# Kernel tuning notes

Hardware: AMD Instinct MI355X
Metric: run time of the kernel (lower is better)

The kernel has to match this reference:

```python
import jax, jax.numpy as jnp
import numpy as np

H = 1024   # hidden_size
NH = 32    # num_heads
D = H // NH  # head_dim = 32
M = 2      # num_timescales
BMIN, BMAX = 0.85, 0.9995
EPS = 1e-6
ROPE_BASE = 10000.0
LN_EPS = 1e-5


def setup_inputs() -> dict:
    key = jax.random.key(0)
    ks = jax.random.split(key, 8)
    b, t = 4, 1024
    x = jax.random.normal(ks[0], (b, t, H), jnp.float32)
    # xavier-uniform for q/k/v/out (matches _reset_parameters)
    sc = (6.0 / (H + H)) ** 0.5
    Wq = jax.random.uniform(ks[1], (H, H), jnp.float32, -sc, sc)
    Wk = jax.random.uniform(ks[2], (H, H), jnp.float32, -sc, sc)
    Wv = jax.random.uniform(ks[3], (H, H), jnp.float32, -sc, sc)
    Wout = jax.random.uniform(ks[4], (H, H), jnp.float32, -sc, sc)
    bout = jnp.zeros((H,), jnp.float32)
    # beta_proj: random weight, bias set so sigmoid(bias) = linspace(beta_min, beta_max)
    scb = (6.0 / (H + NH * M)) ** 0.5
    Wbeta = jax.random.uniform(ks[5], (NH * M, H), jnp.float32, -scb, scb)
    targets = jnp.linspace(BMIN, BMAX, M)
    bbeta = jnp.tile(jnp.log(targets / (1.0 - targets)), NH)  # repeat 'm -> (h m)'
    # mix_proj initialized to zeros (uniform mixing via softmax)
    Wmix = jnp.zeros((NH * M, H), jnp.float32)
    bmix = jnp.zeros((NH * M,), jnp.float32)
    ln_g = jnp.ones((H,), jnp.float32)
    ln_b = jnp.zeros((H,), jnp.float32)
    return dict(x=x, Wq=Wq, Wk=Wk, Wv=Wv, Wbeta=Wbeta, bbeta=bbeta,
                Wmix=Wmix, bmix=bmix, Wout=Wout, bout=bout, ln_g=ln_g, ln_b=ln_b)


def _rope(u, cos, sin):
    # u: [b,t,h,d] with d even; cos/sin: [1,t,1,d//2]
    half = D // 2
    u1, u2 = u[..., :half], u[..., half:]
    return jnp.concatenate([u1 * cos - u2 * sin, u1 * sin + u2 * cos], axis=-1)


def _forward(x, Wq, Wk, Wv, Wbeta, bbeta, Wmix, bmix, Wout, bout, ln_g, ln_b):
    b, t, _ = x.shape
    q = (x @ Wq.T).reshape(b, t, NH, D)
    k = (x @ Wk.T).reshape(b, t, NH, D)
    v = (x @ Wv.T).reshape(b, t, NH, D)
    # RoPE cache
    half = D // 2
    inv_freq = 1.0 / (ROPE_BASE ** (jnp.arange(half, dtype=jnp.float32) / half))
    freqs = jnp.arange(t, dtype=jnp.float32)[:, None] * inv_freq  # [t,half]
    cos = jnp.cos(freqs)[None, :, None, :]
    sin = jnp.sin(freqs)[None, :, None, :]
    q = _rope(q, cos, sin)
    k = _rope(k, cos, sin)
    phi_q = jax.nn.elu(q) + 1.0
    phi_k = jax.nn.elu(k) + 1.0
    beta = jnp.clip(jax.nn.sigmoid((x @ Wbeta.T + bbeta).reshape(b, t, NH, M)), BMIN, BMAX)
    mix = jax.nn.softmax((x @ Wmix.T + bmix).reshape(b, t, NH, M), axis=-1)

    def step(carry, xs):
        S, K = carry  # S:[b,h,M,d,d]  K:[b,h,M,d]
        pq, pk, vt, bt, mt = xs  # [b,h,d],[b,h,d],[b,h,d],[b,h,M],[b,h,M]
        K = K * bt[..., None] + pk[:, :, None, :]
        S = S * bt[..., None, None] + pk[:, :, None, :, None] * vt[:, :, None, None, :]
        num = jnp.einsum('bhd,bhmdc->bhmc', pq, S)
        den = jnp.einsum('bhd,bhmd->bhm', pq, K) + EPS
        y = jnp.sum(num / den[..., None] * mt[..., None], axis=2)  # [b,h,d]
        return (S, K), y

    S0 = jnp.zeros((b, NH, M, D, D), x.dtype)
    K0 = jnp.zeros((b, NH, M, D), x.dtype)
    tf = lambda a: jnp.moveaxis(a, 1, 0)  # time-major for scan
    _, ys = jax.lax.scan(step, (S0, K0), (tf(phi_q), tf(phi_k), tf(v), tf(beta), tf(mix)))
    y = jnp.moveaxis(ys, 0, 1).reshape(b, t, H) @ Wout.T + bout
    z = x + y  # residual; dropout is identity in eval
    mu = z.mean(-1, keepdims=True)
    var = ((z - mu) ** 2).mean(-1, keepdims=True)
    return (z - mu) / jnp.sqrt(var + LN_EPS) * ln_g + ln_b


def reference(x, Wq, Wk, Wv, Wbeta, bbeta, Wmix, bmix, Wout, bout, ln_g, ln_b):
    return _forward(x, Wq, Wk, Wv, Wbeta, bbeta, Wmix, bmix, Wout, bout, ln_g, ln_b)
```

## Files before the change

### kernel.cpp

```cpp
#include <hip/hip_runtime.h>
#include <math.h>

#define TT 1024
#define BB 4
#define HH 1024
#define NHH 32
#define CL 64
#define NCH (TT/CL)

typedef unsigned short u16;
typedef __attribute__((ext_vector_type(8))) short short8;
typedef __attribute__((ext_vector_type(8))) unsigned short u16x8;
typedef __attribute__((ext_vector_type(4))) float floatx4;

__device__ __forceinline__ float sigmoidf_(float x){ return 1.f/(1.f+expf(-x)); }
__device__ __forceinline__ u16 f2b(float f){
  union { float f; unsigned u; } x; x.f = f;
  unsigned r = x.u + 0x7FFFu + ((x.u >> 16) & 1u);
  return (u16)(r >> 16);
}
__device__ __forceinline__ float b2f(u16 v){
  union { unsigned u; float f; } x; x.u = ((unsigned)v) << 16;
  return x.f;
}

__global__ __launch_bounds__(256) void cast_all_k(
    const float* __restrict__ x, const float* __restrict__ Wq, const float* __restrict__ Wk,
    const float* __restrict__ Wv, const float* __restrict__ Wbeta, const float* __restrict__ Wmix,
    const float* __restrict__ Wout,
    u16* __restrict__ x_bf, u16* __restrict__ Wf, u16* __restrict__ Wout_bf)
{
  size_t e = ((size_t)blockIdx.x*256 + threadIdx.x)*4;
  const float* src; u16* dst; size_t so, dof;
  if      (e < 4194304) { src=x;     dst=x_bf;    so=e;          dof=so; }
  else if (e < 5242880) { src=Wq;    dst=Wf;      so=e-4194304;  dof=so; }
  else if (e < 6291456) { src=Wk;    dst=Wf;      so=e-5242880;  dof=so+1048576; }
  else if (e < 7340032) { src=Wv;    dst=Wf;      so=e-6291456;  dof=so+2097152; }
  else if (e < 7405568) { src=Wbeta; dst=Wf;      so=e-7340032;  dof=so+3145728; }
  else if (e < 7471104) { src=Wmix;  dst=Wf;      so=e-7405568;  dof=so+3211264; }
  else                  { src=Wout;  dst=Wout_bf; so=e-7471104;  dof=so; }
  float4 f = *reinterpret_cast<const float4*>(src + so);
  ushort4 u; u.x=f2b(f.x); u.y=f2b(f.y); u.z=f2b(f.z); u.w=f2b(f.w);
  *reinterpret_cast<ushort4*>(dst + dof) = u;
}

__global__ __launch_bounds__(256) void rope_table_k(float* __restrict__ ct, float* __restrict__ st){
  int idx = blockIdx.x*256 + threadIdx.x;
  int t = idx >> 4, j = idx & 15;
  float invf = powf(10000.f, -(float)j/16.f);
  float ang = (float)t * invf;
  ct[idx] = cosf(ang);
  st[idx] = sinf(ang);
}

__global__ __launch_bounds__(256) void gemm_qkv_k(
    const u16* __restrict__ A, const u16* __restrict__ W,
    const float* __restrict__ ct, const float* __restrict__ st,
    u16* __restrict__ qkv, float* __restrict__ bmraw)
{
  __shared__ u16 As[128*64];
  __shared__ u16 Ws[128*64];
  const int tid = threadIdx.x;
  const int lane = tid & 63;
  const int wave = tid >> 6;
  const int wm = wave >> 1, wn = wave & 1;
  const int row0 = blockIdx.y*128, col0 = blockIdx.x*128;
  const int lr = lane & 15, lkg = lane >> 4;

  floatx4 acc[4][4];
  #pragma unroll
  for (int mt=0; mt<4; ++mt)
    #pragma unroll
    for (int nt=0; nt<4; ++nt)
      acc[mt][nt] = (floatx4){0.f,0.f,0.f,0.f};

  for (int k0 = 0; k0 < 1024; k0 += 64) {
    __syncthreads();
    #pragma unroll
    for (int it = 0; it < 4; ++it) {
      int li  = it*256 + tid;
      int row = li >> 3, ckp = li & 7;
      int ck  = ckp ^ (row & 7);
      const u16* ga = A + (size_t)(row0+row)*1024 + k0 + ck*8;
      const u16* gw = W + (size_t)(col0+row)*1024 + k0 + ck*8;
      __builtin_amdgcn_global_load_lds(
          (const __attribute__((address_space(1))) void*)ga,
          (__attribute__((address_space(3))) void*)(As + (size_t)(li & ~63)*8), 16, 0, 0);
      __builtin_amdgcn_global_load_lds(
          (const __attribute__((address_space(1))) void*)gw,
          (__attribute__((address_space(3))) void*)(Ws + (size_t)(li & ~63)*8), 16, 0, 0);
    }
    __syncthreads();
    #pragma unroll
    for (int kk = 0; kk < 64; kk += 32) {
      short8 af[4], wf[4];
      const int ckw = (kk >> 3) + lkg;
      #pragma unroll
      for (int t = 0; t < 4; ++t) {
        int rowA = wm*64 + t*16 + lr;
        int rowW = wn*64 + t*16 + lr;
        af[t] = *reinterpret_cast<const short8*>(As + rowA*64 + (ckw ^ (rowA & 7))*8);
        wf[t] = *reinterpret_cast<const short8*>(Ws + rowW*64 + (ckw ^ (rowW & 7))*8);
      }
      #pragma unroll
      for (int mt = 0; mt < 4; ++mt)
        #pragma unroll
        for (int nt = 0; nt < 4; ++nt)
          acc[mt][nt] = __builtin_amdgcn_mfma_f32_16x16x32_bf16(af[mt], wf[nt], acc[mt][nt], 0, 0, 0);
    }
  }
  const int bx = blockIdx.x;
  if (bx < 16) {
    #pragma unroll
    for (int mt = 0; mt < 4; ++mt) {
      #pragma unroll
      for (int r = 0; r < 4; ++r) {
        int row = row0 + wm*64 + mt*16 + lkg*4 + r;
        int t = row & (TT-1);
        float c_ = ct[t*16 + lr], s_ = st[t*16 + lr];
        #pragma unroll
        for (int nt = 0; nt < 4; nt += 2) {
          float u1 = acc[mt][nt][r], u2 = acc[mt][nt+1][r];
          float r1 = u1*c_ - u2*s_;
          float r2 = u1*s_ + u2*c_;
          r1 = r1 > 0.f ? r1+1.f : expf(r1);
          r2 = r2 > 0.f ? r2+1.f : expf(r2);
          int col = col0 + wn*64 + nt*16 + lr;
          qkv[(size_t)row*3072 + col]      = f2b(r1);
          qkv[(size_t)row*3072 + col + 16] = f2b(r2);
        }
      }
    }
  } else if (bx < 24) {
    #pragma unroll
    for (int mt = 0; mt < 4; ++mt)
      #pragma unroll
      for (int r = 0; r < 4; ++r) {
        int row = row0 + wm*64 + mt*16 + lkg*4 + r;
        #pragma unroll
        for (int nt = 0; nt < 4; ++nt) {
          int col = col0 + wn*64 + nt*16 + lr;
          qkv[(size_t)row*3072 + col] = f2b(acc[mt][nt][r]);
        }
      }
  } else {
    #pragma unroll
    for (int mt = 0; mt < 4; ++mt)
      #pragma unroll
      for (int r = 0; r < 4; ++r) {
        int row = row0 + wm*64 + mt*16 + lkg*4 + r;
        #pragma unroll
        for (int nt = 0; nt < 4; ++nt) {
          int col = col0 + wn*64 + nt*16 + lr - 3072;
          bmraw[(size_t)row*128 + col] = acc[mt][nt][r];
        }
      }
  }
}

__global__ __launch_bounds__(256) void gemm_mfma_k(
    const u16* __restrict__ A, const u16* __restrict__ W,
    const float* __restrict__ bias, const float* __restrict__ res,
    float* __restrict__ Cf, int N, int K)
{
  __shared__ u16 As[128*64];
  __shared__ u16 Ws[128*64];
  const int tid = threadIdx.x;
  const int lane = tid & 63;
  const int wave = tid >> 6;
  const int wm = wave >> 1, wn = wave & 1;
  const int row0 = blockIdx.y*128, col0 = blockIdx.x*128;
  const int lr = lane & 15, lkg = lane >> 4;
  floatx4 acc[4][4];
  #pragma unroll
  for (int mt=0; mt<4; ++mt)
    #pragma unroll
    for (int nt=0; nt<4; ++nt)
      acc[mt][nt] = (floatx4){0.f,0.f,0.f,0.f};
  for (int k0 = 0; k0 < K; k0 += 64) {
    __syncthreads();
    #pragma unroll
    for (int it = 0; it < 4; ++it) {
      int li  = it*256 + tid;
      int row = li >> 3, ckp = li & 7;
      int ck  = ckp ^ (row & 7);
      const u16* ga = A + (size_t)(row0+row)*K + k0 + ck*8;
      const u16* gw = W + (size_t)(col0+row)*K + k0 + ck*8;
      __builtin_amdgcn_global_load_lds(
          (const __attribute__((address_space(1))) void*)ga,
          (__attribute__((address_space(3))) void*)(As + (size_t)(li & ~63)*8), 16, 0, 0);
      __builtin_amdgcn_global_load_lds(
          (const __attribute__((address_space(1))) void*)gw,
          (__attribute__((address_space(3))) void*)(Ws + (size_t)(li & ~63)*8), 16, 0, 0);
    }
    __syncthreads();
    #pragma unroll
    for (int kk = 0; kk < 64; kk += 32) {
      short8 af[4], wf[4];
      const int ckw = (kk >> 3) + lkg;
      #pragma unroll
      for (int t = 0; t < 4; ++t) {
        int rowA = wm*64 + t*16 + lr;
        int rowW = wn*64 + t*16 + lr;
        af[t] = *reinterpret_cast<const short8*>(As + rowA*64 + (ckw ^ (rowA & 7))*8);
        wf[t] = *reinterpret_cast<const short8*>(Ws + rowW*64 + (ckw ^ (rowW & 7))*8);
      }
      #pragma unroll
      for (int mt = 0; mt < 4; ++mt)
        #pragma unroll
        for (int nt = 0; nt < 4; ++nt)
          acc[mt][nt] = __builtin_amdgcn_mfma_f32_16x16x32_bf16(af[mt], wf[nt], acc[mt][nt], 0, 0, 0);
    }
  }
  #pragma unroll
  for (int mt = 0; mt < 4; ++mt) {
    #pragma unroll
    for (int r = 0; r < 4; ++r) {
      int row = row0 + wm*64 + mt*16 + lkg*4 + r;
      #pragma unroll
      for (int nt = 0; nt < 4; ++nt) {
        int col = col0 + wn*64 + nt*16 + lr;
        float v = acc[mt][nt][r];
        if (bias) v += bias[col];
        if (res)  v += res[(size_t)row*N + col];
        Cf[(size_t)row*N + col] = v;
      }
    }
  }
}

__global__ __launch_bounds__(256) void scan_delta_k(
    const u16* __restrict__ qkv, const float* __restrict__ bmraw,
    const float* __restrict__ bbeta,
    float* __restrict__ dS, float* __restrict__ dK,
    float* __restrict__ pLg, float* __restrict__ pg)
{
  __shared__ __align__(16) u16 K2T[2][32][72];
  __shared__ __align__(16) u16 VT[32][72];
  __shared__ float bets[2][64], pbuf[2][64], wjs[2][64], pLs[2];
  const int ch = blockIdx.x, h = blockIdx.y, b = blockIdx.z;
  const int bh = b*NHH + h;
  const int tid = threadIdx.x;
  const int t0 = ch*CL;
  const int j = tid >> 2, oct = tid & 3;
  size_t rowbase = (size_t)(b*TT + t0 + j)*3072 + h*32 + oct*8;
  u16x8 k8 = *reinterpret_cast<const u16x8*>(qkv + rowbase + 1024);
  u16x8 v8 = *reinterpret_cast<const u16x8*>(qkv + rowbase + 2048);
  if (tid < 128) {
    int m = tid & 1, tl = tid >> 1;
    float bv = bmraw[(size_t)(b*TT + t0 + tl)*128 + h*2 + m] + bbeta[h*2 + m];
    bets[m][tl] = fminf(fmaxf(sigmoidf_(bv), 0.85f), 0.9995f);
  }
  #pragma unroll
  for (int dd = 0; dd < 8; ++dd) VT[oct*8+dd][j] = v8[dd];
  __syncthreads();
  if (tid < 128) {
    int m = tid >> 6, l = tid & 63;
    float p = bets[m][l];
    #pragma unroll
    for (int off = 1; off < 64; off <<= 1) {
      float o = __shfl_up(p, off);
      if (l >= off) p *= o;
    }
    pbuf[m][l] = p;
    if (l == 63) pLs[m] = p;
  }
  __syncthreads();
  if (tid < 128) {
    int m = tid >> 6, l = tid & 63;
    wjs[m][l] = pLs[m] / pbuf[m][l];
    pg[(((size_t)bh*NCH + ch)*2 + m)*64 + l] = pbuf[m][l];
  }
  if (tid < 2) pLg[((size_t)bh*NCH + ch)*2 + tid] = pLs[tid];
  __syncthreads();
  float w0 = wjs[0][j], w1 = wjs[1][j];
  #pragma unroll
  for (int dd = 0; dd < 8; ++dd) {
    float kv = b2f(k8[dd]);
    K2T[0][oct*8+dd][j] = f2b(kv*w0);
    K2T[1][oct*8+dd][j] = f2b(kv*w1);
  }
  __syncthreads();
  {
    const int wv = tid >> 6, lane = tid & 63, lr = lane & 15, kg = lane >> 4;
    const int m = wv >> 1, mt = wv & 1;
    floatx4 a0 = (floatx4){0.f,0.f,0.f,0.f}, a1 = (floatx4){0.f,0.f,0.f,0.f};
    #pragma unroll
    for (int ks = 0; ks < 2; ++ks) {
      short8 af = *reinterpret_cast<const short8*>(&K2T[m][mt*16 + lr][ks*32 + kg*8]);
      short8 b0 = *reinterpret_cast<const short8*>(&VT[lr][ks*32 + kg*8]);
      short8 b1 = *reinterpret_cast<const short8*>(&VT[16 + lr][ks*32 + kg*8]);
      a0 = __builtin_amdgcn_mfma_f32_16x16x32_bf16(af, b0, a0, 0, 0, 0);
      a1 = __builtin_amdgcn_mfma_f32_16x16x32_bf16(af, b1, a1, 0, 0, 0);
    }
    size_t base = (((size_t)bh*NCH + ch)*2 + m)*1024;
    #pragma unroll
    for (int r = 0; r < 4; ++r) {
      int d = mt*16 + kg*4 + r;
      dS[base + d*32 + lr]      = a0[r];
      dS[base + d*32 + 16 + lr] = a1[r];
    }
  }
  if (tid < 64) {
    int m = tid >> 5, d = tid & 31;
    float s = 0.f;
    #pragma unroll
    for (int g = 0; g < 8; ++g) {
      u16x8 kk = *reinterpret_cast<const u16x8*>(&K2T[m][d][g*8]);
      #pragma unroll
      for (int dd = 0; dd < 8; ++dd) s += b2f(kk[dd]);
    }
    dK[(((size_t)bh*NCH + ch)*2 + m)*32 + d] = s;
  }
}

__global__ __launch_bounds__(1024) void scan_state_k(
    float* dSS0, float* dKK0, const float* __restrict__ pLg)
{
  const int bhm = blockIdx.x;
  const int bh = bhm >> 1, m = bhm & 1;
  const int tid = threadIdx.x;
  float pls[NCH], dv[NCH];
  #pragma unroll
  for (int ch = 0; ch < NCH; ++ch) pls[ch] = pLg[((size_t)bh*NCH + ch)*2 + m];
  #pragma unroll
  for (int ch = 0; ch < NCH; ++ch) dv[ch] = dSS0[(((size_t)bh*NCH + ch)*2 + m)*1024 + tid];
  float S = 0.f;
  #pragma unroll
  for (int ch = 0; ch < NCH; ++ch) {
    dSS0[(((size_t)bh*NCH + ch)*2 + m)*1024 + tid] = S;
    S = fmaf(pls[ch], S, dv[ch]);
  }
  if (tid < 32) {
    float kv[NCH];
    #pragma unroll
    for (int ch = 0; ch < NCH; ++ch) kv[ch] = dKK0[(((size_t)bh*NCH + ch)*2 + m)*32 + tid];
    float K0 = 0.f;
    #pragma unroll
    for (int ch = 0; ch < NCH; ++ch) {
      dKK0[(((size_t)bh*NCH + ch)*2 + m)*32 + tid] = K0;
      K0 = fmaf(pls[ch], K0, kv[ch]);
    }
  }
}

__global__ __launch_bounds__(256) void scan_apply_k(
    const u16* __restrict__ qkv, const float* __restrict__ bmraw,
    const float* __restrict__ bmix,
    const float* __restrict__ S0g, const float* __restrict__ K0g,
    const float* __restrict__ pg, u16* __restrict__ yb)
{
  __shared__ __align__(16) u16 Qs[64][32], Ks[64][32];
  __shared__ __align__(16) u16 VT[32][72];
  __shared__ __align__(16) u16 At[2][64][72];
  __shared__ __align__(16) u16 S0T[2][2][32][40];
  __shared__ float K0s[2][32];
  __shared__ float pbv[2][64], ipb[2][64], mixs[2][64], coef[2][64];
  const int ch = blockIdx.x, h = blockIdx.y, b = blockIdx.z;
  const int bh = b*NHH + h;
  const int tid = threadIdx.x;
  const int t0 = ch*CL;
  {
    int j = tid >> 2, oct = tid & 3;
    size_t rb = (size_t)(b*TT + t0 + j)*3072 + h*32 + oct*8;
    u16x8 q8 = *reinterpret_cast<const u16x8*>(qkv + rb);
    u16x8 k8 = *reinterpret_cast<const u16x8*>(qkv + rb + 1024);
    u16x8 v8 = *reinterpret_cast<const u16x8*>(qkv + rb + 2048);
    *reinterpret_cast<u16x8*>(&Qs[j][oct*8]) = q8;
    *reinterpret_cast<u16x8*>(&Ks[j][oct*8]) = k8;
    #pragma unroll
    for (int dd = 0; dd < 8; ++dd) VT[oct*8+dd][j] = v8[dd];
  }
  for (int u = tid; u < 2048; u += 256) {
    int m = u >> 10, r = u & 1023, d = r >> 5, c = r & 31;
    float val = S0g[(((size_t)bh*NCH + ch)*2 + m)*1024 + r];
    u16 hv = f2b(val);
    float lo = val - b2f(hv);
    S0T[m][0][c][d] = hv;
    S0T[m][1][c][d] = f2b(lo);
  }
  if (tid < 64) {
    int m = tid >> 5, d = tid & 31;
    K0s[m][d] = K0g[(((size_t)bh*NCH + ch)*2 + m)*32 + d];
  }
  if (tid < 128) {
    int m = tid & 1, i = tid >> 1;
    float p = pg[(((size_t)bh*NCH + ch)*2 + m)*64 + i];
    pbv[m][i] = p;
    ipb[m][i] = 1.f/p;
  } else if (tid < 192) {
    int i = tid - 128;
    size_t rb = (size_t)(b*TT + t0 + i)*128 + 64 + h*2;
    float a0 = bmraw[rb]   + bmix[h*2];
    float a1 = bmraw[rb+1] + bmix[h*2+1];
    float mx = fmaxf(a0, a1);
    float e0 = expf(a0-mx), e1 = expf(a1-mx);
    float inv = 1.f/(e0+e1);
    mixs[0][i] = e0*inv; mixs[1][i] = e1*inv;
  }
  __syncthreads();
  {
    const int wv = tid >> 6, lane = tid & 63, lr = lane & 15, kg = lane >> 4;
    short8 aq = *reinterpret_cast<const short8*>(&Qs[wv*16 + lr][kg*8]);
    #pragma unroll
    for (int nt = 0; nt < 4; ++nt) {
      short8 bk = *reinterpret_cast<const short8*>(&Ks[nt*16 + lr][kg*8]);
      floatx4 a0 = (floatx4){0.f,0.f,0.f,0.f};
      a0 = __builtin_amdgcn_mfma_f32_16x16x32_bf16(aq, bk, a0, 0, 0, 0);
      int jg = nt*16 + lr;
      float ip0 = ipb[0][jg], ip1 = ipb[1][jg];
      #pragma unroll
      for (int r = 0; r < 4; ++r) {
        int ig = wv*16 + kg*4 + r;
        float val = a0[r];
        bool ok = (jg <= ig);
        At[0][ig][jg] = f2b(ok ? val*ip0 : 0.f);
        At[1][ig][jg] = f2b(ok ? val*ip1 : 0.f);
      }
    }
  }
  __syncthreads();
  if (tid < 128) {
    int m = tid & 1, i = tid >> 1;
    float qK0 = 0.f;
    #pragma unroll
    for (int g = 0; g < 4; ++g) {
      u16x8 qq = *reinterpret_cast<const u16x8*>(&Qs[i][g*8]);
      #pragma unroll
      for (int dd = 0; dd < 8; ++dd) qK0 = fmaf(b2f(qq[dd]), K0s[m][g*8+dd], qK0);
    }
    float As_ = 0.f;
    #pragma unroll
    for (int g = 0; g < 8; ++g) {
      u16x8 aa = *reinterpret_cast<const u16x8*>(&At[m][i][g*8]);
      #pragma unroll
      for (int dd = 0; dd < 8; ++dd) As_ += b2f(aa[dd]);
    }
    float den = pbv[m][i]*(qK0 + As_) + 1e-6f;
    coef[m][i] = mixs[m][i]*pbv[m][i]/den;
  }
  __syncthreads();
  {
    const int wv = tid >> 6, lane = tid & 63, lr = lane & 15, kg = lane >> 4;
    const int i0 = wv*16;
    floatx4 accY[2][2];
    #pragma unroll
    for (int m = 0; m < 2; ++m)
      #pragma unroll
      for (int nt = 0; nt < 2; ++nt)
        accY[m][nt] = (floatx4){0.f,0.f,0.f,0.f};
    short8 aq = *reinterpret_cast<const short8*>(&Qs[i0 + lr][kg*8]);
    #pragma unroll
    for (int m = 0; m < 2; ++m)
      #pragma unroll
      for (int nt = 0; nt < 2; ++nt) {
        short8 bhi = *reinterpret_cast<const short8*>(&S0T[m][0][nt*16 + lr][kg*8]);
        short8 blo = *reinterpret_cast<const short8*>(&S0T[m][1][nt*16 + lr][kg*8]);
        accY[m][nt] = __builtin_amdgcn_mfma_f32_16x16x32_bf16(aq, bhi, accY[m][nt], 0, 0, 0);
        accY[m][nt] = __builtin_amdgcn_mfma_f32_16x16x32_bf16(aq, blo, accY[m][nt], 0, 0, 0);
      }
    #pragma unroll
    for (int ks = 0; ks < 2; ++ks) {
      short8 a0f = *reinterpret_cast<const short8*>(&At[0][i0 + lr][ks*32 + kg*8]);
      short8 a1f = *reinterpret_cast<const short8*>(&At[1][i0 + lr][ks*32 + kg*8]);
      short8 b0 = *reinterpret_cast<const short8*>(&VT[lr][ks*32 + kg*8]);
      short8 b1 = *reinterpret_cast<const short8*>(&VT[16 + lr][ks*32 + kg*8]);
      accY[0][0] = __builtin_amdgcn_mfma_f32_16x16x32_bf16(a0f, b0, accY[0][0], 0, 0, 0);
      accY[0][1] = __builtin_amdgcn_mfma_f32_16x16x32_bf16(a0f, b1, accY[0][1], 0, 0, 0);
      accY[1][0] = __builtin_amdgcn_mfma_f32_16x16x32_bf16(a1f, b0, accY[1][0], 0, 0, 0);
      accY[1][1] = __builtin_amdgcn_mfma_f32_16x16x32_bf16(a1f, b1, accY[1][1], 0, 0, 0);
    }
    #pragma unroll
    for (int r = 0; r < 4; ++r) {
      int i = i0 + kg*4 + r;
      float c0 = coef[0][i], c1 = coef[1][i];
      size_t ob = (size_t)(b*TT + t0 + i)*HH + h*32;
      yb[ob + lr]      = f2b(c0*accY[0][0][r] + c1*accY[1][0][r]);
      yb[ob + 16 + lr] = f2b(c0*accY[0][1][r] + c1*accY[1][1][r]);
    }
  }
}

__global__ __launch_bounds__(256) void ln_k(
    const float* __restrict__ z, const float* __restrict__ g,
    const float* __restrict__ bta, float* __restrict__ out)
{
  const int row = blockIdx.x;
  const int tid = threadIdx.x;
  const float* zr = z + (size_t)row*HH;
  float4 zv = reinterpret_cast<const float4*>(zr)[tid];
  float sum = zv.x+zv.y+zv.z+zv.w;
  float sq  = zv.x*zv.x + zv.y*zv.y + zv.z*zv.z + zv.w*zv.w;
  #pragma unroll
  for (int off=1; off<64; off<<=1){ sum += __shfl_xor(sum, off); sq += __shfl_xor(sq, off); }
  __shared__ float s1[4], s2[4];
  int w = tid>>6;
  if ((tid&63)==0){ s1[w]=sum; s2[w]=sq; }
  __syncthreads();
  sum = s1[0]+s1[1]+s1[2]+s1[3];
  sq  = s2[0]+s2[1]+s2[2]+s2[3];
  float mu  = sum * (1.f/1024.f);
  float var = sq * (1.f/1024.f) - mu*mu;
  float rstd = rsqrtf(var + 1e-5f);
  float4 gv = reinterpret_cast<const float4*>(g)[tid];
  float4 bv = reinterpret_cast<const float4*>(bta)[tid];
  float4 ov;
  ov.x = (zv.x-mu)*rstd*gv.x + bv.x;
  ov.y = (zv.y-mu)*rstd*gv.y + bv.y;
  ov.z = (zv.z-mu)*rstd*gv.z + bv.z;
  ov.w = (zv.w-mu)*rstd*gv.w + bv.w;
  reinterpret_cast<float4*>(out + (size_t)row*HH)[tid] = ov;
}

extern "C" void kernel_launch(void* const* d_in, const int* in_sizes, int n_in,
                              void* d_out, int out_size, void* d_ws, size_t ws_size,
                              hipStream_t stream)
{
  const float* x     = (const float*)d_in[0];
  const float* Wq    = (const float*)d_in[1];
  const float* Wk    = (const float*)d_in[2];
  const float* Wv    = (const float*)d_in[3];
  const float* Wbeta = (const float*)d_in[4];
  const float* bbeta = (const float*)d_in[5];
  const float* Wmix  = (const float*)d_in[6];
  const float* bmix  = (const float*)d_in[7];
  const float* Wout  = (const float*)d_in[8];
  const float* bout  = (const float*)d_in[9];
  const float* ln_g  = (const float*)d_in[10];
  const float* ln_b  = (const float*)d_in[11];
  float* out = (float*)d_out;

  float* ws = (float*)d_ws;
  float* ct      = ws;
  float* st      = ws + 16384;
  u16*   x_bf    = (u16*)(ws + 32768);
  u16*   Wf      = (u16*)(ws + 2129920);
  u16*   Wout_bf = (u16*)(ws + 3768320);
  u16*   qkv     = (u16*)(ws + 4292608);
  float* bmraw   = ws + 10584064;
  float* dSS0    = ws + 11108352;
  float* dKK0    = ws + 15302656;
  float* pLg     = ws + 15433728;
  float* pg      = ws + 15437824;
  u16*   y_bf    = x_bf;
  float* z       = dSS0;

  cast_all_k<<<8320, 256, 0, stream>>>(x, Wq, Wk, Wv, Wbeta, Wmix, Wout, x_bf, Wf, Wout_bf);
  rope_table_k<<<64, 256, 0, stream>>>(ct, st);
  gemm_qkv_k<<<dim3(25, 32), 256, 0, stream>>>(x_bf, Wf, ct, st, qkv, bmraw);
  dim3 gscan(NCH, 32, 4);
  scan_delta_k<<<gscan, 256, 0, stream>>>(qkv, bmraw, bbeta, dSS0, dKK0, pLg, pg);
  scan_state_k<<<256, 1024, 0, stream>>>(dSS0, dKK0, pLg);
  scan_apply_k<<<gscan, 256, 0, stream>>>(qkv, bmraw, bmix, dSS0, dKK0, pg, y_bf);
  gemm_mfma_k<<<dim3(8, 32), 256, 0, stream>>>(y_bf, Wout_bf, bout, x, z, 1024, 1024);
  ln_k<<<4096, 256, 0, stream>>>(z, ln_g, ln_b, out);
}
```

Before: 237.9 us.

## Fuse rope table into cast, split-K output GEMM, fold beta/mix into QKV epilogue

Merges the RoPE table kernel into the cast kernel, and computes beta sigmoid/clamp and the mix softmax in the QKV GEMM epilogue instead of in the scan kernels. The output projection is split-K into two halves writing separate partial buffers, and the residual, bias and partial sums are combined inside the layernorm kernel. It also reorders the GEMM block indexing into a 1D grid with row-fastest order and splits scan_state into 256-thread blocks. This removes one launch and redundant per-chunk beta/mix math, and doubles output-GEMM block count for better CU occupancy, at the cost of extra partial-buffer traffic.

```diff
diff --git a/kernel.cpp b/kernel.cpp
--- a/kernel.cpp
+++ b/kernel.cpp
@@ -28,9 +28,18 @@
     const float* __restrict__ x, const float* __restrict__ Wq, const float* __restrict__ Wk,
     const float* __restrict__ Wv, const float* __restrict__ Wbeta, const float* __restrict__ Wmix,
     const float* __restrict__ Wout,
-    u16* __restrict__ x_bf, u16* __restrict__ Wf, u16* __restrict__ Wout_bf)
-{
-  size_t e = ((size_t)blockIdx.x*256 + threadIdx.x)*4;
+    u16* __restrict__ x_bf, u16* __restrict__ Wf, u16* __restrict__ Wout_bf,
+    float* __restrict__ ct, float* __restrict__ st)
+{
+  int gid = blockIdx.x*256 + threadIdx.x;
+  if (gid < 16384) {
+    int t = gid >> 4, j = gid & 15;
+    float invf = powf(10000.f, -(float)j/16.f);
+    float ang = (float)t * invf;
+    ct[gid] = cosf(ang);
+    st[gid] = sinf(ang);
+  }
+  size_t e = (size_t)gid*4;
   const float* src; u16* dst; size_t so, dof;
   if      (e < 4194304) { src=x;     dst=x_bf;    so=e;          dof=so; }
   else if (e < 5242880) { src=Wq;    dst=Wf;      so=e-4194304;  dof=so; }
@@ -44,19 +53,11 @@
   *reinterpret_cast<ushort4*>(dst + dof) = u;
 }
 
-__global__ __launch_bounds__(256) void rope_table_k(float* __restrict__ ct, float* __restrict__ st){
-  int idx = blockIdx.x*256 + threadIdx.x;
-  int t = idx >> 4, j = idx & 15;
-  float invf = powf(10000.f, -(float)j/16.f);
-  float ang = (float)t * invf;
-  ct[idx] = cosf(ang);
-  st[idx] = sinf(ang);
-}
-
 __global__ __launch_bounds__(256) void gemm_qkv_k(
     const u16* __restrict__ A, const u16* __restrict__ W,
     const float* __restrict__ ct, const float* __restrict__ st,
-    u16* __restrict__ qkv, float* __restrict__ bmraw)
+    const float* __restrict__ bbeta, const float* __restrict__ bmix,
+    u16* __restrict__ qkv, float* __restrict__ betag, float* __restrict__ mixg)
 {
   __shared__ u16 As[128*64];
   __shared__ u16 Ws[128*64];
@@ -64,7 +65,8 @@
   const int lane = tid & 63;
   const int wave = tid >> 6;
   const int wm = wave >> 1, wn = wave & 1;
-  const int row0 = blockIdx.y*128, col0 = blockIdx.x*128;
+  const int id = blockIdx.x;
+  const int row0 = (id & 31)*128, bx = id >> 5, col0 = bx*128;
   const int lr = lane & 15, lkg = lane >> 4;
 
   floatx4 acc[4][4];
@@ -109,7 +111,6 @@
           acc[mt][nt] = __builtin_amdgcn_mfma_f32_16x16x32_bf16(af[mt], wf[nt], acc[mt][nt], 0, 0, 0);
     }
   }
-  const int bx = blockIdx.x;
   if (bx < 16) {
     #pragma unroll
     for (int mt = 0; mt < 4; ++mt) {
@@ -151,17 +152,26 @@
         int row = row0 + wm*64 + mt*16 + lkg*4 + r;
         #pragma unroll
         for (int nt = 0; nt < 4; ++nt) {
-          int col = col0 + wn*64 + nt*16 + lr - 3072;
-          bmraw[(size_t)row*128 + col] = acc[mt][nt][r];
+          int cidx = nt*16 + lr;
+          float v = acc[mt][nt][r];
+          if (wn == 0) {
+            float bv = sigmoidf_(v + bbeta[cidx]);
+            betag[(size_t)row*64 + cidx] = fminf(fmaxf(bv, 0.85f), 0.9995f);
+          } else {
+            float a = v + bmix[cidx];
+            float o = __shfl_xor(a, 1);
+            float e = expf(a - fmaxf(a, o));
+            float es = e + __shfl_xor(e, 1);
+            mixg[(size_t)row*64 + cidx] = e/es;
+          }
         }
       }
   }
 }
 
-__global__ __launch_bounds__(256) void gemm_mfma_k(
+__global__ __launch_bounds__(256) void gemm_out_k(
     const u16* __restrict__ A, const u16* __restrict__ W,
-    const float* __restrict__ bias, const float* __restrict__ res,
-    float* __restrict__ Cf, int N, int K)
+    float* __restrict__ Zp0, float* __restrict__ Zp1)
 {
   __shared__ u16 As[128*64];
   __shared__ u16 Ws[128*64];
@@ -169,7 +179,9 @@
   const int lane = tid & 63;
   const int wave = tid >> 6;
   const int wm = wave >> 1, wn = wave & 1;
-  const int row0 = blockIdx.y*128, col0 = blockIdx.x*128;
+  const int id = blockIdx.x;
+  const int row0 = (id & 31)*128, col0 = ((id >> 5) & 7)*128, kh = id >> 8;
+  float* Z = kh ? Zp1 : Zp0;
   const int lr = lane & 15, lkg = lane >> 4;
   floatx4 acc[4][4];
   #pragma unroll
@@ -177,15 +189,15 @@
     #pragma unroll
     for (int nt=0; nt<4; ++nt)
       acc[mt][nt] = (floatx4){0.f,0.f,0.f,0.f};
-  for (int k0 = 0; k0 < K; k0 += 64) {
+  for (int k0 = kh*512; k0 < kh*512 + 512; k0 += 64) {
     __syncthreads();
     #pragma unroll
     for (int it = 0; it < 4; ++it) {
       int li  = it*256 + tid;
       int row = li >> 3, ckp = li & 7;
       int ck  = ckp ^ (row & 7);
-      const u16* ga = A + (size_t)(row0+row)*K + k0 + ck*8;
-      const u16* gw = W + (size_t)(col0+row)*K + k0 + ck*8;
+      const u16* ga = A + (size_t)(row0+row)*1024 + k0 + ck*8;
+      const u16* gw = W + (size_t)(col0+row)*1024 + k0 + ck*8;
       __builtin_amdgcn_global_load_lds(
           (const __attribute__((address_space(1))) void*)ga,
           (__attribute__((address_space(3))) void*)(As + (size_t)(li & ~63)*8), 16, 0, 0);
@@ -213,25 +225,20 @@
     }
   }
   #pragma unroll
-  for (int mt = 0; mt < 4; ++mt) {
+  for (int mt = 0; mt < 4; ++mt)
     #pragma unroll
     for (int r = 0; r < 4; ++r) {
       int row = row0 + wm*64 + mt*16 + lkg*4 + r;
       #pragma unroll
       for (int nt = 0; nt < 4; ++nt) {
         int col = col0 + wn*64 + nt*16 + lr;
-        float v = acc[mt][nt][r];
-        if (bias) v += bias[col];
-        if (res)  v += res[(size_t)row*N + col];
-        Cf[(size_t)row*N + col] = v;
-      }
-    }
-  }
+        Z[(size_t)row*HH + col] = acc[mt][nt][r];
+      }
+    }
 }
 
 __global__ __launch_bounds__(256) void scan_delta_k(
-    const u16* __restrict__ qkv, const float* __restrict__ bmraw,
-    const float* __restrict__ bbeta,
+    const u16* __restrict__ qkv, const float* __restrict__ betag,
     float* __restrict__ dS, float* __restrict__ dK,
     float* __restrict__ pLg, float* __restrict__ pg)
 {
@@ -248,8 +255,7 @@
   u16x8 v8 = *reinterpret_cast<const u16x8*>(qkv + rowbase + 2048);
   if (tid < 128) {
     int m = tid & 1, tl = tid >> 1;
-    float bv = bmraw[(size_t)(b*TT + t0 + tl)*128 + h*2 + m] + bbeta[h*2 + m];
-    bets[m][tl] = fminf(fmaxf(sigmoidf_(bv), 0.85f), 0.9995f);
+    bets[m][tl] = betag[(size_t)(b*TT + t0 + tl)*64 + h*2 + m];
   }
   #pragma unroll
   for (int dd = 0; dd < 8; ++dd) VT[oct*8+dd][j] = v8[dd];
@@ -314,39 +320,39 @@
   }
 }
 
-__global__ __launch_bounds__(1024) void scan_state_k(
+__global__ __launch_bounds__(256) void scan_state_k(
     float* dSS0, float* dKK0, const float* __restrict__ pLg)
 {
-  const int bhm = blockIdx.x;
+  const int bhm = blockIdx.x >> 2, part = blockIdx.x & 3;
   const int bh = bhm >> 1, m = bhm & 1;
-  const int tid = threadIdx.x;
+  const int idx = part*256 + threadIdx.x;
   float pls[NCH], dv[NCH];
   #pragma unroll
   for (int ch = 0; ch < NCH; ++ch) pls[ch] = pLg[((size_t)bh*NCH + ch)*2 + m];
   #pragma unroll
-  for (int ch = 0; ch < NCH; ++ch) dv[ch] = dSS0[(((size_t)bh*NCH + ch)*2 + m)*1024 + tid];
+  for (int ch = 0; ch < NCH; ++ch) dv[ch] = dSS0[(((size_t)bh*NCH + ch)*2 + m)*1024 + idx];
   float S = 0.f;
   #pragma unroll
   for (int ch = 0; ch < NCH; ++ch) {
-    dSS0[(((size_t)bh*NCH + ch)*2 + m)*1024 + tid] = S;
+    dSS0[(((size_t)bh*NCH + ch)*2 + m)*1024 + idx] = S;
     S = fmaf(pls[ch], S, dv[ch]);
   }
-  if (tid < 32) {
+  if (part == 0 && threadIdx.x < 32) {
+    int d = threadIdx.x;
     float kv[NCH];
     #pragma unroll
-    for (int ch = 0; ch < NCH; ++ch) kv[ch] = dKK0[(((size_t)bh*NCH + ch)*2 + m)*32 + tid];
+    for (int ch = 0; ch < NCH; ++ch) kv[ch] = dKK0[(((size_t)bh*NCH + ch)*2 + m)*32 + d];
     float K0 = 0.f;
     #pragma unroll
     for (int ch = 0; ch < NCH; ++ch) {
-      dKK0[(((size_t)bh*NCH + ch)*2 + m)*32 + tid] = K0;
+      dKK0[(((size_t)bh*NCH + ch)*2 + m)*32 + d] = K0;
       K0 = fmaf(pls[ch], K0, kv[ch]);
     }
   }
 }
 
 __global__ __launch_bounds__(256) void scan_apply_k(
-    const u16* __restrict__ qkv, const float* __restrict__ bmraw,
-    const float* __restrict__ bmix,
+    const u16* __restrict__ qkv, const float* __restrict__ mixg,
     const float* __restrict__ S0g, const float* __restrict__ K0g,
     const float* __restrict__ pg, u16* __restrict__ yb)
 {
@@ -390,13 +396,9 @@
     ipb[m][i] = 1.f/p;
   } else if (tid < 192) {
     int i = tid - 128;
-    size_t rb = (size_t)(b*TT + t0 + i)*128 + 64 + h*2;
-    float a0 = bmraw[rb]   + bmix[h*2];
-    float a1 = bmraw[rb+1] + bmix[h*2+1];
-    float mx = fmaxf(a0, a1);
-    float e0 = expf(a0-mx), e1 = expf(a1-mx);
-    float inv = 1.f/(e0+e1);
-    mixs[0][i] = e0*inv; mixs[1][i] = e1*inv;
+    size_t rb = (size_t)(b*TT + t0 + i)*64 + h*2;
+    mixs[0][i] = mixg[rb];
+    mixs[1][i] = mixg[rb+1];
   }
   __syncthreads();
   {
@@ -482,13 +484,22 @@
 }
 
 __global__ __launch_bounds__(256) void ln_k(
-    const float* __restrict__ z, const float* __restrict__ g,
+    const float* __restrict__ xr, const float* __restrict__ zp0, const float* __restrict__ zp1,
+    const float* __restrict__ bout, const float* __restrict__ g,
     const float* __restrict__ bta, float* __restrict__ out)
 {
   const int row = blockIdx.x;
   const int tid = threadIdx.x;
-  const float* zr = z + (size_t)row*HH;
-  float4 zv = reinterpret_cast<const float4*>(zr)[tid];
+  size_t o = (size_t)row*HH/4 + tid;
+  float4 xv = reinterpret_cast<const float4*>(xr)[o];
+  float4 z0 = reinterpret_cast<const float4*>(zp0)[o];
+  float4 z1 = reinterpret_cast<const float4*>(zp1)[o];
+  float4 bo = reinterpret_cast<const float4*>(bout)[tid];
+  float4 zv;
+  zv.x = xv.x + z0.x + z1.x + bo.x;
+  zv.y = xv.y + z0.y + z1.y + bo.y;
+  zv.z = xv.z + z0.z + z1.z + bo.z;
+  zv.w = xv.w + z0.w + z1.w + bo.w;
   float sum = zv.x+zv.y+zv.z+zv.w;
   float sq  = zv.x*zv.x + zv.y*zv.y + zv.z*zv.z + zv.w*zv.w;
   #pragma unroll
@@ -509,7 +520,7 @@
   ov.y = (zv.y-mu)*rstd*gv.y + bv.y;
   ov.z = (zv.z-mu)*rstd*gv.z + bv.z;
   ov.w = (zv.w-mu)*rstd*gv.w + bv.w;
-  reinterpret_cast<float4*>(out + (size_t)row*HH)[tid] = ov;
+  reinterpret_cast<float4*>(out)[o] = ov;
 }
 
 extern "C" void kernel_launch(void* const* d_in, const int* in_sizes, int n_in,
@@ -537,21 +548,23 @@
   u16*   Wf      = (u16*)(ws + 2129920);
   u16*   Wout_bf = (u16*)(ws + 3768320);
   u16*   qkv     = (u16*)(ws + 4292608);
-  float* bmraw   = ws + 10584064;
+  float* betag   = ws + 10584064;
+  float* mixg    = ws + 10846208;
   float* dSS0    = ws + 11108352;
   float* dKK0    = ws + 15302656;
   float* pLg     = ws + 15433728;
   float* pg      = ws + 15437824;
   u16*   y_bf    = x_bf;
-  float* z       = dSS0;
-
-  cast_all_k<<<8320, 256, 0, stream>>>(x, Wq, Wk, Wv, Wbeta, Wmix, Wout, x_bf, Wf, Wout_bf);
-  rope_table_k<<<64, 256, 0, stream>>>(ct, st);
-  gemm_qkv_k<<<dim3(25, 32), 256, 0, stream>>>(x_bf, Wf, ct, st, qkv, bmraw);
+  float* zp0     = dSS0;
+  float* zp1     = (float*)qkv;
+
+  cast_all_k<<<8320, 256, 0, stream>>>(x, Wq, Wk, Wv, Wbeta, Wmix, Wout,
+                                       x_bf, Wf, Wout_bf, ct, st);
+  gemm_qkv_k<<<800, 256, 0, stream>>>(x_bf, Wf, ct, st, bbeta, bmix, qkv, betag, mixg);
   dim3 gscan(NCH, 32, 4);
-  scan_delta_k<<<gscan, 256, 0, stream>>>(qkv, bmraw, bbeta, dSS0, dKK0, pLg, pg);
-  scan_state_k<<<256, 1024, 0, stream>>>(dSS0, dKK0, pLg);
-  scan_apply_k<<<gscan, 256, 0, stream>>>(qkv, bmraw, bmix, dSS0, dKK0, pg, y_bf);
-  gemm_mfma_k<<<dim3(8, 32), 256, 0, stream>>>(y_bf, Wout_bf, bout, x, z, 1024, 1024);
-  ln_k<<<4096, 256, 0, stream>>>(z, ln_g, ln_b, out);
-}
+  scan_delta_k<<<gscan, 256, 0, stream>>>(qkv, betag, dSS0, dKK0, pLg, pg);
+  scan_state_k<<<1024, 256, 0, stream>>>(dSS0, dKK0, pLg);
+  scan_apply_k<<<gscan, 256, 0, stream>>>(qkv, mixg, dSS0, dKK0, pg, y_bf);
+  gemm_out_k<<<512, 256, 0, stream>>>(y_bf, Wout_bf, zp0, zp1);
+  ln_k<<<4096, 256, 0, stream>>>(x, zp0, zp1, bout, ln_g, ln_b, out);
+}
```

Measured after the change: 224.4 us. 1.06x faster.
